# Performance work log

Measured on AMD Instinct MI355X. Metric: run time of the kernel, lower is better.

Reference implementation:

```python
import jax, jax.numpy as jnp
import numpy as np

B, T, C, H = 2, 2048, 1024, 16
D = C // H  # head_dim = 64


def _ln(x, g, b, eps=1e-5):
    mu = x.mean(-1, keepdims=True)
    var = ((x - mu) ** 2).mean(-1, keepdims=True)
    return (x - mu) / jnp.sqrt(var + eps) * g + b


def _lif_rate(I, tau_rc=0.02, tau_ref=0.002, v_th=1.0, eps=1e-7):
    good = I > v_th + eps
    I_safe = jnp.where(good, I, v_th + 1.0)  # avoid log1p(<=-1)
    r = 1.0 / (tau_ref - tau_rc * jnp.log1p(-v_th / I_safe))
    return jnp.where(good, r, 0.0)


def setup_inputs() -> dict:
    key = jax.random.key(0)
    ks = jax.random.split(key, 12)
    w = lambda k, shp: jax.random.normal(k, shp, dtype=jnp.float32) * 0.02
    enc = jax.random.normal(ks[9], (H, T, D), dtype=jnp.float32)
    enc_hat = enc / jnp.maximum(jnp.linalg.norm(enc, axis=-1, keepdims=True), 1e-8)
    return {
        "x": jax.random.normal(ks[0], (B, T, C), dtype=jnp.float32),
        "ln1_g": jnp.ones((C,), jnp.float32), "ln1_b": jnp.zeros((C,), jnp.float32),
        "qkv_w": w(ks[1], (C, 3 * C)), "qkv_b": jnp.zeros((3 * C,), jnp.float32),
        "out_w": w(ks[2], (C, C)), "out_b": jnp.zeros((C,), jnp.float32),
        "ln2_g": jnp.ones((C,), jnp.float32), "ln2_b": jnp.zeros((C,), jnp.float32),
        "mlp_w1": w(ks[3], (C, 4 * C)), "mlp_b1": jnp.zeros((4 * C,), jnp.float32),
        "mlp_w2": w(ks[4], (4 * C, C)), "mlp_b2": jnp.zeros((C,), jnp.float32),
        "enc_hat": enc_hat,
        "gain": jax.random.uniform(ks[10], (1, H, T, 1), dtype=jnp.float32) * 200.0,
        "bias_attn": jax.random.uniform(ks[11], (1, H, T, 1), dtype=jnp.float32),
    }


def reference(x, ln1_g, ln1_b, qkv_w, qkv_b, out_w, out_b,
              ln2_g, ln2_b, mlp_w1, mlp_b1, mlp_w2, mlp_b2,
              enc_hat, gain, bias_attn):
    b, t, c = x.shape
    x_norm = _ln(x, ln1_g, ln1_b)
    qkv = x_norm @ qkv_w + qkv_b                      # [B,T,3C]
    qkv = qkv.reshape(b, t, 3, H, D).transpose(2, 0, 3, 1, 4)
    Q, K_unused, V = qkv[0], qkv[1], qkv[2]           # each [B,H,T,D]; K unused (matches source)
    E = enc_hat[:, :t, :]
    G = gain[:, :, :t, :]
    BIAS = bias_attn[:, :, :t, :]
    I = G * jnp.einsum('bhtd,hsd->bhts', Q, E) + BIAS  # [B,H,T,T]
    scores = _lif_rate(I) / jnp.sqrt(jnp.float32(D))
    causal = jnp.tril(jnp.ones((t, t), dtype=bool))[None, None]
    scores = jnp.where(causal, scores, -jnp.inf)
    attn_w = jax.nn.softmax(scores, axis=-1)
    attn_out = jnp.einsum('bhts,bhsd->bhtd', attn_w, V)
    attn_out = attn_out.transpose(0, 2, 1, 3).reshape(b, t, c)
    x = x + attn_out @ out_w + out_b
    h = _ln(x, ln2_g, ln2_b)
    h = jax.nn.gelu(h @ mlp_w1 + mlp_b1, approximate=False) @ mlp_w2 + mlp_b2
    return x + h
```

## Files before the change

kernel.cpp:

```cpp
#include <hip/hip_runtime.h>
#include <math.h>

#define Bdim 2
#define Tdim 2048
#define Cdim 1024
#define Hdim 16
#define Ddim 64

typedef unsigned short u16;
typedef __attribute__((ext_vector_type(8))) short bf16x8;
typedef __attribute__((ext_vector_type(4))) float f32x4;

__device__ __forceinline__ float b2f(u16 s){
  union { float f; unsigned u; } v; v.u = ((unsigned)s) << 16; return v.f;
}
__device__ __forceinline__ u16 f2b(float f){
  union { float f; unsigned u; } v; v.f = f;
  unsigned r = v.u + 0x7fffu + ((v.u >> 16) & 1u);
  return (u16)(r >> 16);
}
__device__ __forceinline__ float loadf(const void* p, size_t i, int bf){
  float r;
  if(bf) r = b2f(((const u16*)p)[i]);
  else   r = ((const float*)p)[i];
  return r;
}
__device__ __forceinline__ f32x4 mfma16(bf16x8 a, bf16x8 b, f32x4 c){
  return __builtin_amdgcn_mfma_f32_16x16x32_bf16(a, b, c, 0, 0, 0);
}
__device__ __forceinline__ void glds16(const u16* g, u16* l){
  __builtin_amdgcn_global_load_lds(
      (const __attribute__((address_space(1))) unsigned int*)g,
      (__attribute__((address_space(3))) unsigned int*)l, 16, 0, 0);
}

__global__ void detect_k(const u16* __restrict__ x, int* __restrict__ flag){
  if(threadIdx.x == 0 && blockIdx.x == 0){
    int sane = 0;
    for(int i = 0; i < 64; i++){
      int e = (x[i] >> 7) & 0xFF;
      sane += (e == 0 || (e >= 0x6E && e <= 0x8A)) ? 1 : 0;
    }
    *flag = (sane >= 56) ? 1 : 0;
  }
}

__global__ __launch_bounds__(256) void cvt_k(const void* __restrict__ in,
    u16* __restrict__ out, int n, const int* __restrict__ flagp){
  int bf = *flagp;
  int i = blockIdx.x * 256 + threadIdx.x;
  if(i < n) out[i] = bf ? ((const u16*)in)[i] : f2b(((const float*)in)[i]);
}

__global__ __launch_bounds__(256) void transpose_k(const void* __restrict__ in,
    u16* __restrict__ out, int K, int N, const int* __restrict__ flagp){
  __shared__ u16 tile[32][34];
  int bf = *flagp;
  int n0 = blockIdx.x * 32, k0 = blockIdx.y * 32;
  int tx = threadIdx.x & 31, ty = threadIdx.x >> 5;
  #pragma unroll
  for(int i = 0; i < 4; i++)
    tile[ty + i*8][tx] = f2b(loadf(in, (size_t)(k0 + ty + i*8) * N + n0 + tx, bf));
  __syncthreads();
  #pragma unroll
  for(int i = 0; i < 4; i++)
    out[(size_t)(n0 + ty + i*8) * K + k0 + tx] = tile[tx][ty + i*8];
}

template<int SRC>
__global__ __launch_bounds__(256) void ln_k(const void* __restrict__ xin,
    const void* __restrict__ g, const void* __restrict__ be,
    u16* __restrict__ out, const int* __restrict__ flagp){
  __shared__ float red[256];
  int bf = *flagp;
  int row = blockIdx.x, t = threadIdx.x;
  float v[4]; float s = 0.f;
  #pragma unroll
  for(int i = 0; i < 4; i++){
    size_t idx = (size_t)row * Cdim + t + i*256;
    v[i] = (SRC == 1) ? ((const float*)xin)[idx] : loadf(xin, idx, bf);
    s += v[i];
  }
  red[t] = s; __syncthreads();
  for(int o = 128; o > 0; o >>= 1){ if(t < o) red[t] += red[t+o]; __syncthreads(); }
  float mu = red[0] * (1.f / Cdim);
  __syncthreads();
  s = 0.f;
  #pragma unroll
  for(int i = 0; i < 4; i++){ float d = v[i] - mu; s += d*d; }
  red[t] = s; __syncthreads();
  for(int o = 128; o > 0; o >>= 1){ if(t < o) red[t] += red[t+o]; __syncthreads(); }
  float rstd = rsqrtf(red[0] * (1.f / Cdim) + 1e-5f);
  u16* orow = out + (size_t)row * Cdim;
  #pragma unroll
  for(int i = 0; i < 4; i++){
    int c = t + i*256;
    orow[c] = f2b((v[i] - mu) * rstd * loadf(g, c, bf) + loadf(be, c, bf));
  }
}

enum { EPI_QKV = 0, EPI_RES = 1, EPI_GELU = 2, EPI_FINAL = 3 };

template<int EPI, int KK>
__global__ __launch_bounds__(256) void gemm_k(
    const u16* __restrict__ A, const u16* __restrict__ Bt, const void* __restrict__ bias,
    void* __restrict__ out0, void* __restrict__ out1, const void* __restrict__ res,
    int M, int N, int mofs, const int* __restrict__ flagp)
{
  const int K = KK;
  __shared__ u16 As[128 * 64];
  __shared__ u16 Bs[128 * 64];
  int bf = *flagp;
  int tid = threadIdx.x;
  int m0 = blockIdx.y * 128, n0 = blockIdx.x * 128;
  int w = tid >> 6, l = tid & 63;
  int lq = l & 15, lk = l >> 4;
  int m_off = (w & 1) * 64, n_off = (w >> 1) * 64;
  int grow = w * 32 + (l >> 3);
  int gcol = (l & 7) * 8;
  const u16* Ab = A + (size_t)(m0 + grow) * K + gcol;
  const u16* Bb;
  {
    int brow = n0 + grow;
    if(EPI == EPI_QKV && n0 >= 1024) brow += 1024;
    Bb = Bt + (size_t)brow * K + gcol;
  }
  u16* Asw = &As[(size_t)(w * 32) * 64];
  u16* Bsw = &Bs[(size_t)(w * 32) * 64];
  f32x4 acc[4][4] = {};
  for(int k0 = 0; k0 < K; k0 += 64){
    __syncthreads();
    #pragma unroll
    for(int i = 0; i < 4; i++)
      glds16(Ab + (size_t)(i*8) * K + k0, Asw + i*8*64);
    #pragma unroll
    for(int i = 0; i < 4; i++)
      glds16(Bb + (size_t)(i*8) * K + k0, Bsw + i*8*64);
    __syncthreads();
    #pragma unroll
    for(int kk = 0; kk < 2; kk++){
      bf16x8 af[4], bfr[4];
      #pragma unroll
      for(int mb = 0; mb < 4; mb++)
        af[mb]  = *(const bf16x8*)&As[(m_off + mb*16 + lq) * 64 + kk*32 + lk*8];
      #pragma unroll
      for(int nb = 0; nb < 4; nb++)
        bfr[nb] = *(const bf16x8*)&Bs[(n_off + nb*16 + lq) * 64 + kk*32 + lk*8];
      #pragma unroll
      for(int mb = 0; mb < 4; mb++)
        #pragma unroll
        for(int nb = 0; nb < 4; nb++)
          acc[mb][nb] = mfma16(af[mb], bfr[nb], acc[mb][nb]);
    }
  }
  #pragma unroll
  for(int mb = 0; mb < 4; mb++)
  #pragma unroll
  for(int nb = 0; nb < 4; nb++){
    #pragma unroll
    for(int r = 0; r < 4; r++){
      int m = m0 + m_off + mb*16 + lk*4 + r;
      int n = n0 + n_off + nb*16 + lq;
      float v = acc[mb][nb][r];
      if(EPI == EPI_QKV){
        int bsrc = (n < 1024) ? n : n + 1024;
        v += loadf(bias, bsrc, bf);
        int bb = m / Tdim, t = m % Tdim;
        if(n < 1024){
          int h = n >> 6, d = n & 63;
          ((u16*)out0)[(((size_t)(bb*Hdim + h)*Tdim + t) << 6) + d] = f2b(v);
        } else {
          int nv = n - 1024; int h = nv >> 6, d = nv & 63;
          ((u16*)out1)[((size_t)(bb*Hdim + h)*Ddim + d)*Tdim + t] = f2b(v);
        }
      } else if(EPI == EPI_RES){
        v += loadf(bias, n, bf) + loadf(res, (size_t)m*N + n, bf);
        ((float*)out0)[(size_t)m*N + n] = v;
      } else if(EPI == EPI_GELU){
        v += loadf(bias, n, bf);
        float gl = 0.5f * v * (1.0f + erff(v * 0.70710678118f));
        ((u16*)out0)[(size_t)m*N + n] = f2b(gl);
      } else {
        v += loadf(bias, n, bf) + ((const float*)res)[(size_t)m*N + n];
        size_t oi = (size_t)(mofs + m) * N + n;
        if(bf) ((u16*)out0)[oi] = f2b(v);
        else   ((float*)out0)[oi] = v;
      }
    }
  }
}

__global__ __launch_bounds__(256, 3) void attn_k(
    const u16* __restrict__ Q, const u16* __restrict__ Vt, const u16* __restrict__ E,
    const void* __restrict__ gain, const void* __restrict__ battn,
    u16* __restrict__ aout, const int* __restrict__ flagp)
{
  __shared__ u16 Es[2][64][72];
  __shared__ u16 Vs[2][64][72];
  __shared__ u16 P[4][16][72];
  int bf = *flagp;
  int k  = 31 - (int)(blockIdx.x >> 5);
  int bh = blockIdx.x & 31;
  int b = bh >> 4, h = bh & 15;
  int tid = threadIdx.x;
  int w = tid >> 6, l = tid & 63;
  int lq = l & 15, lk = l >> 4;
  int rt = k * 4 + w;
  int qrow = rt * 16;
  const u16* Qb = Q  + (size_t)bh * Tdim * Ddim;
  const u16* Vb = Vt + (size_t)bh * Ddim * Tdim;
  const u16* Eh = E  + (size_t)h  * Tdim * Ddim;
  int srow = tid >> 3;
  int scol = (tid & 7) * 8;
  bf16x8 qf[2];
  #pragma unroll
  for(int ks = 0; ks < 2; ks++)
    qf[ks] = *(const bf16x8*)(Qb + (size_t)(qrow + lq) * Ddim + ks*32 + lk*8);
  float g4[4], b4[4];
  #pragma unroll
  for(int r = 0; r < 4; r++){
    int t = qrow + lk*4 + r;
    g4[r] = loadf(gain, h * Tdim + t, bf);
    b4[r] = loadf(battn, h * Tdim + t, bf);
  }
  bf16x8 onesf;
  #pragma unroll
  for(int j = 0; j < 8; j++) onesf[j] = (short)0x3F80;
  f32x4 num[4] = {};
  f32x4 den4 = {0.f, 0.f, 0.f, 0.f};
  {
    bf16x8 e0 = *(const bf16x8*)(Eh + (size_t)(srow     ) * Ddim + scol);
    bf16x8 e1 = *(const bf16x8*)(Eh + (size_t)(srow + 32) * Ddim + scol);
    bf16x8 v0 = *(const bf16x8*)(Vb + (size_t)(srow     ) * Tdim + scol);
    bf16x8 v1 = *(const bf16x8*)(Vb + (size_t)(srow + 32) * Tdim + scol);
    *(bf16x8*)&Es[0][srow     ][scol] = e0;
    *(bf16x8*)&Es[0][srow + 32][scol] = e1;
    *(bf16x8*)&Vs[0][srow     ][scol] = v0;
    *(bf16x8*)&Vs[0][srow + 32][scol] = v1;
  }
  __syncthreads();
  for(int st = 0; st <= k; st++){
    int cur = st & 1;
    bf16x8 pe0, pe1, pv0, pv1;
    if(st < k){
      pe0 = *(const bf16x8*)(Eh + (size_t)((st+1)*64 + srow     ) * Ddim + scol);
      pe1 = *(const bf16x8*)(Eh + (size_t)((st+1)*64 + srow + 32) * Ddim + scol);
      pv0 = *(const bf16x8*)(Vb + (size_t)(srow     ) * Tdim + (st+1)*64 + scol);
      pv1 = *(const bf16x8*)(Vb + (size_t)(srow + 32) * Tdim + (st+1)*64 + scol);
    }
    f32x4 sc[4] = {};
    #pragma unroll
    for(int ks = 0; ks < 2; ks++){
      #pragma unroll
      for(int nb = 0; nb < 4; nb++){
        bf16x8 ef = *(const bf16x8*)&Es[cur][nb*16 + lq][ks*32 + lk*8];
        sc[nb] = mfma16(qf[ks], ef, sc[nb]);
      }
    }
    int diag = (st == k);
    #pragma unroll
    for(int nb = 0; nb < 4; nb++){
      #pragma unroll
      for(int r = 0; r < 4; r++){
        int sg = st*64 + nb*16 + lq;
        int qg = qrow + lk*4 + r;
        float I = fmaf(g4[r], sc[nb][r], b4[r]);
        float u = (I - 1.0f) * __builtin_amdgcn_rcpf(I);
        float L = __builtin_amdgcn_logf(u);
        float denom = fmaf(-0.013862944f, L, 0.002f);
        float e = __builtin_amdgcn_exp2f(0.18033688f * __builtin_amdgcn_rcpf(denom));
        float p = (I > 1.0000001f) ? e : 1.0f;
        if(diag) p = (sg <= qg) ? p : 0.f;
        P[w][lk*4 + r][nb*16 + lq] = f2b(p);
      }
    }
    #pragma unroll
    for(int ks = 0; ks < 2; ks++){
      bf16x8 pf = *(const bf16x8*)&P[w][lq][ks*32 + lk*8];
      den4 = mfma16(pf, onesf, den4);
      #pragma unroll
      for(int nb = 0; nb < 4; nb++){
        bf16x8 vf = *(const bf16x8*)&Vs[cur][nb*16 + lq][ks*32 + lk*8];
        num[nb] = mfma16(pf, vf, num[nb]);
      }
    }
    if(st < k){
      *(bf16x8*)&Es[cur^1][srow     ][scol] = pe0;
      *(bf16x8*)&Es[cur^1][srow + 32][scol] = pe1;
      *(bf16x8*)&Vs[cur^1][srow     ][scol] = pv0;
      *(bf16x8*)&Vs[cur^1][srow + 32][scol] = pv1;
      __syncthreads();
    }
  }
  float rden[4];
  #pragma unroll
  for(int r = 0; r < 4; r++) rden[r] = __builtin_amdgcn_rcpf(den4[r]);
  #pragma unroll
  for(int nb = 0; nb < 4; nb++){
    #pragma unroll
    for(int r = 0; r < 4; r++){
      int t = qrow + lk*4 + r;
      int d = nb*16 + lq;
      float o = num[nb][r] * rden[r];
      aout[((size_t)b * Tdim + t) * Cdim + h * Ddim + d] = f2b(o);
    }
  }
}

extern "C" void kernel_launch(void* const* d_in, const int* in_sizes, int n_in,
                              void* d_out, int out_size, void* d_ws, size_t ws_size,
                              hipStream_t stream)
{
  const void* x      = d_in[0];
  const void* ln1_g  = d_in[1];
  const void* ln1_b  = d_in[2];
  const void* qkv_w  = d_in[3];
  const void* qkv_b  = d_in[4];
  const void* out_w  = d_in[5];
  const void* out_b  = d_in[6];
  const void* ln2_g  = d_in[7];
  const void* ln2_b  = d_in[8];
  const void* mlp_w1 = d_in[9];
  const void* mlp_b1 = d_in[10];
  const void* mlp_w2 = d_in[11];
  const void* mlp_b2 = d_in[12];
  const void* enc    = d_in[13];
  const void* gain   = d_in[14];
  const void* battn  = d_in[15];
  (void)in_sizes; (void)n_in; (void)out_size;

  const size_t MB = 1024 * 1024;
  char* ws = (char*)d_ws;
  int*   flag = (int*)(ws);
  u16*   R0   = (u16*)(ws + 256);
  u16*   R1   = (u16*)(ws + 256 + 8*MB);
  float* x2   = (float*)(ws + 256 + 16*MB);
  u16*   R3a  = (u16*)(ws + 256 + 32*MB);
  u16*   R3b  = (u16*)(ws + 256 + 40*MB);
  u16*   Ebf  = (u16*)(ws + 256 + 48*MB);
  u16*   gbuf = (u16*)(ws + 256 + 52*MB);
  bool fullM = ws_size >= 85*MB;

  dim3 blk(256);
  detect_k<<<1, 64, 0, stream>>>((const u16*)x, flag);
  ln_k<0><<<4096, blk, 0, stream>>>(x, ln1_g, ln1_b, R0, flag);
  transpose_k<<<dim3(3072/32, 1024/32), blk, 0, stream>>>(qkv_w, R1, 1024, 3072, flag);
  cvt_k<<<(Hdim*Tdim*Ddim)/256, blk, 0, stream>>>(enc, Ebf, Hdim*Tdim*Ddim, flag);
  gemm_k<EPI_QKV,1024><<<dim3(2048/128, 4096/128), blk, 0, stream>>>(
      R0, R1, qkv_b, R3a, R3b, nullptr, 4096, 2048, 0, flag);
  attn_k<<<dim3(32*32), dim3(256), 0, stream>>>(R3a, R3b, Ebf, gain, battn, R0, flag);
  transpose_k<<<dim3(1024/32, 1024/32), blk, 0, stream>>>(out_w, R1, 1024, 1024, flag);
  gemm_k<EPI_RES,1024><<<dim3(1024/128, 4096/128), blk, 0, stream>>>(
      R0, R1, out_b, x2, nullptr, x, 4096, 1024, 0, flag);
  ln_k<1><<<4096, blk, 0, stream>>>(x2, ln2_g, ln2_b, R3a, flag);
  transpose_k<<<dim3(4096/32, 1024/32), blk, 0, stream>>>(mlp_w1, R0, 1024, 4096, flag);
  transpose_k<<<dim3(1024/32, 4096/32), blk, 0, stream>>>(mlp_w2, R1, 4096, 1024, flag);
  if(fullM){
    gemm_k<EPI_GELU,1024><<<dim3(4096/128, 4096/128), blk, 0, stream>>>(
        R3a, R0, mlp_b1, gbuf, nullptr, nullptr, 4096, 4096, 0, flag);
    gemm_k<EPI_FINAL,4096><<<dim3(1024/128, 4096/128), blk, 0, stream>>>(
        gbuf, R1, mlp_b2, d_out, nullptr, x2, 4096, 1024, 0, flag);
  } else {
    for(int q = 0; q < 4; q++){
      int ro = q * 1024;
      gemm_k<EPI_GELU,1024><<<dim3(4096/128, 1024/128), blk, 0, stream>>>(
          R3a + (size_t)ro*1024, R0, mlp_b1, R3b, nullptr, nullptr, 1024, 4096, 0, flag);
      gemm_k<EPI_FINAL,4096><<<dim3(1024/128, 1024/128), blk, 0, stream>>>(
          R3b, R1, mlp_b2, d_out, nullptr, x2 + (size_t)ro*1024, 1024, 1024, ro, flag);
    }
  }
}
```

Before: 492.7 us.

## Double-buffer GEMM shared-memory tiles and XOR-swizzle LDS layout

Adds an optional double-buffered main loop to the bf16 MFMA GEMM, so the next K-tile loads into the second LDS buffer while the current one is computed. This removes one barrier per iteration and overlaps global-to-LDS traffic with MFMA work. It also XOR-swizzles the 16-byte column chunks on store and load to cut LDS bank conflicts on fragment reads. Double buffering is enabled only for the output projection, the final MLP GEMM and the chunked GELU path. It doubles LDS per block on those launches, which may lower occupancy.

```diff
diff --git a/kernel.cpp b/kernel.cpp
--- a/kernel.cpp
+++ b/kernel.cpp
@@ -101,15 +101,15 @@
 
 enum { EPI_QKV = 0, EPI_RES = 1, EPI_GELU = 2, EPI_FINAL = 3 };
 
-template<int EPI, int KK>
+template<int EPI, int KK, int DBUF>
 __global__ __launch_bounds__(256) void gemm_k(
     const u16* __restrict__ A, const u16* __restrict__ Bt, const void* __restrict__ bias,
     void* __restrict__ out0, void* __restrict__ out1, const void* __restrict__ res,
     int M, int N, int mofs, const int* __restrict__ flagp)
 {
   const int K = KK;
-  __shared__ u16 As[128 * 64];
-  __shared__ u16 Bs[128 * 64];
+  __shared__ u16 As[(DBUF ? 2 : 1) * 128 * 64];
+  __shared__ u16 Bs[(DBUF ? 2 : 1) * 128 * 64];
   int bf = *flagp;
   int tid = threadIdx.x;
   int m0 = blockIdx.y * 128, n0 = blockIdx.x * 128;
@@ -117,7 +117,7 @@
   int lq = l & 15, lk = l >> 4;
   int m_off = (w & 1) * 64, n_off = (w >> 1) * 64;
   int grow = w * 32 + (l >> 3);
-  int gcol = (l & 7) * 8;
+  int gcol = (((l & 7) ^ ((l >> 3) & 7))) * 8;
   const u16* Ab = A + (size_t)(m0 + grow) * K + gcol;
   const u16* Bb;
   {
@@ -127,32 +127,58 @@
   }
   u16* Asw = &As[(size_t)(w * 32) * 64];
   u16* Bsw = &Bs[(size_t)(w * 32) * 64];
+
+  #define STAGE(buf, k0)                                                   \
+    do{ _Pragma("unroll")                                                  \
+      for(int i = 0; i < 4; i++)                                           \
+        glds16(Ab + (size_t)(i*8) * K + (k0), Asw + (buf)*8192 + i*8*64);  \
+      _Pragma("unroll")                                                    \
+      for(int i = 0; i < 4; i++)                                           \
+        glds16(Bb + (size_t)(i*8) * K + (k0), Bsw + (buf)*8192 + i*8*64);  \
+    } while(0)
+
   f32x4 acc[4][4] = {};
-  for(int k0 = 0; k0 < K; k0 += 64){
+  #define COMPUTE(buf)                                                         \
+    do{ _Pragma("unroll")                                                      \
+      for(int kk = 0; kk < 2; kk++){                                           \
+        bf16x8 af[4], bfr[4];                                                  \
+        _Pragma("unroll")                                                      \
+        for(int mb = 0; mb < 4; mb++)                                          \
+          af[mb]  = *(const bf16x8*)&As[(buf)*8192 +                           \
+              (m_off + mb*16 + lq) * 64 + ((kk*4 + lk) ^ (lq & 7)) * 8];       \
+        _Pragma("unroll")                                                      \
+        for(int nb = 0; nb < 4; nb++)                                          \
+          bfr[nb] = *(const bf16x8*)&Bs[(buf)*8192 +                           \
+              (n_off + nb*16 + lq) * 64 + ((kk*4 + lk) ^ (lq & 7)) * 8];       \
+        _Pragma("unroll")                                                      \
+        for(int mb = 0; mb < 4; mb++)                                          \
+          _Pragma("unroll")                                                    \
+          for(int nb = 0; nb < 4; nb++)                                        \
+            acc[mb][nb] = mfma16(af[mb], bfr[nb], acc[mb][nb]);                \
+      }                                                                        \
+    } while(0)
+
+  if(DBUF){
+    int cur = 0;
+    STAGE(0, 0);
     __syncthreads();
-    #pragma unroll
-    for(int i = 0; i < 4; i++)
-      glds16(Ab + (size_t)(i*8) * K + k0, Asw + i*8*64);
-    #pragma unroll
-    for(int i = 0; i < 4; i++)
-      glds16(Bb + (size_t)(i*8) * K + k0, Bsw + i*8*64);
-    __syncthreads();
-    #pragma unroll
-    for(int kk = 0; kk < 2; kk++){
-      bf16x8 af[4], bfr[4];
-      #pragma unroll
-      for(int mb = 0; mb < 4; mb++)
-        af[mb]  = *(const bf16x8*)&As[(m_off + mb*16 + lq) * 64 + kk*32 + lk*8];
-      #pragma unroll
-      for(int nb = 0; nb < 4; nb++)
-        bfr[nb] = *(const bf16x8*)&Bs[(n_off + nb*16 + lq) * 64 + kk*32 + lk*8];
-      #pragma unroll
-      for(int mb = 0; mb < 4; mb++)
-        #pragma unroll
-        for(int nb = 0; nb < 4; nb++)
-          acc[mb][nb] = mfma16(af[mb], bfr[nb], acc[mb][nb]);
-    }
-  }
+    for(int k0 = 0; k0 < K; k0 += 64){
+      if(k0 + 64 < K) STAGE(cur ^ 1, k0 + 64);
+      COMPUTE(cur);
+      __syncthreads();
+      cur ^= 1;
+    }
+  } else {
+    for(int k0 = 0; k0 < K; k0 += 64){
+      __syncthreads();
+      STAGE(0, k0);
+      __syncthreads();
+      COMPUTE(0);
+    }
+  }
+  #undef STAGE
+  #undef COMPUTE
+
   #pragma unroll
   for(int mb = 0; mb < 4; mb++)
   #pragma unroll
@@ -346,26 +372,26 @@
   ln_k<0><<<4096, blk, 0, stream>>>(x, ln1_g, ln1_b, R0, flag);
   transpose_k<<<dim3(3072/32, 1024/32), blk, 0, stream>>>(qkv_w, R1, 1024, 3072, flag);
   cvt_k<<<(Hdim*Tdim*Ddim)/256, blk, 0, stream>>>(enc, Ebf, Hdim*Tdim*Ddim, flag);
-  gemm_k<EPI_QKV,1024><<<dim3(2048/128, 4096/128), blk, 0, stream>>>(
+  gemm_k<EPI_QKV,1024,0><<<dim3(2048/128, 4096/128), blk, 0, stream>>>(
       R0, R1, qkv_b, R3a, R3b, nullptr, 4096, 2048, 0, flag);
   attn_k<<<dim3(32*32), dim3(256), 0, stream>>>(R3a, R3b, Ebf, gain, battn, R0, flag);
   transpose_k<<<dim3(1024/32, 1024/32), blk, 0, stream>>>(out_w, R1, 1024, 1024, flag);
-  gemm_k<EPI_RES,1024><<<dim3(1024/128, 4096/128), blk, 0, stream>>>(
+  gemm_k<EPI_RES,1024,1><<<dim3(1024/128, 4096/128), blk, 0, stream>>>(
       R0, R1, out_b, x2, nullptr, x, 4096, 1024, 0, flag);
   ln_k<1><<<4096, blk, 0, stream>>>(x2, ln2_g, ln2_b, R3a, flag);
   transpose_k<<<dim3(4096/32, 1024/32), blk, 0, stream>>>(mlp_w1, R0, 1024, 4096, flag);
   transpose_k<<<dim3(1024/32, 4096/32), blk, 0, stream>>>(mlp_w2, R1, 4096, 1024, flag);
   if(fullM){
-    gemm_k<EPI_GELU,1024><<<dim3(4096/128, 4096/128), blk, 0, stream>>>(
+    gemm_k<EPI_GELU,1024,0><<<dim3(4096/128, 4096/128), blk, 0, stream>>>(
         R3a, R0, mlp_b1, gbuf, nullptr, nullptr, 4096, 4096, 0, flag);
-    gemm_k<EPI_FINAL,4096><<<dim3(1024/128, 4096/128), blk, 0, stream>>>(
+    gemm_k<EPI_FINAL,4096,1><<<dim3(1024/128, 4096/128), blk, 0, stream>>>(
         gbuf, R1, mlp_b2, d_out, nullptr, x2, 4096, 1024, 0, flag);
   } else {
     for(int q = 0; q < 4; q++){
       int ro = q * 1024;
-      gemm_k<EPI_GELU,1024><<<dim3(4096/128, 1024/128), blk, 0, stream>>>(
+      gemm_k<EPI_GELU,1024,1><<<dim3(4096/128, 1024/128), blk, 0, stream>>>(
           R3a + (size_t)ro*1024, R0, mlp_b1, R3b, nullptr, nullptr, 1024, 4096, 0, flag);
-      gemm_k<EPI_FINAL,4096><<<dim3(1024/128, 1024/128), blk, 0, stream>>>(
+      gemm_k<EPI_FINAL,4096,1><<<dim3(1024/128, 1024/128), blk, 0, stream>>>(
           R3b, R1, mlp_b2, d_out, nullptr, x2 + (size_t)ro*1024, 1024, 1024, ro, flag);
     }
   }
```

New measurement: 470.7 us. 1.05x faster.
